# Optimization experiments

Hardware: AMD Instinct MI355X
Metric: run time of the kernel (lower is better)

The kernel has to match this reference:

```python
import jax, jax.numpy as jnp
import numpy as np

B, S, D_IN, D_OUT, H = 4, 2048, 1024, 1024, 16
HD = D_OUT // H  # 64


def setup_inputs() -> dict:
    key = jax.random.key(0)
    ks = jax.random.split(key, 6)
    scale_in = 1.0 / np.sqrt(D_IN)
    scale_out = 1.0 / np.sqrt(D_OUT)
    return {
        "x": jax.random.normal(ks[0], (B, S, D_IN), dtype=jnp.float32),
        "Wq": jax.random.normal(ks[1], (D_IN, D_OUT), dtype=jnp.float32) * scale_in,
        "Wk": jax.random.normal(ks[2], (D_IN, D_OUT), dtype=jnp.float32) * scale_in,
        "Wv": jax.random.normal(ks[3], (D_IN, D_OUT), dtype=jnp.float32) * scale_in,
        "Wo": jax.random.normal(ks[4], (D_OUT, D_OUT), dtype=jnp.float32) * scale_out,
        "bo": jax.random.normal(ks[5], (D_OUT,), dtype=jnp.float32) * 0.01,
    }


def reference(x, Wq, Wk, Wv, Wo, bo):
    b, s, _ = x.shape
    # project and split heads: (b, s, d_out) -> (b, h, s, hd)
    def split(t):
        return t.reshape(b, s, H, HD).transpose(0, 2, 1, 3)
    q = split(x @ Wq)
    k = split(x @ Wk)
    v = split(x @ Wv)
    # scaled causal attention scores (b, h, s, s)
    scores = jnp.einsum('bhqd,bhkd->bhqk', q, k) / jnp.sqrt(jnp.float32(HD))
    causal = jnp.tril(jnp.ones((s, s), dtype=bool))
    scores = jnp.where(causal, scores, -jnp.inf)
    weights = jax.nn.softmax(scores, axis=-1)
    # dropout p=0.0 -> identity (eval mode)
    ctx = jnp.einsum('bhqk,bhkd->bhqd', weights, v)
    ctx = ctx.transpose(0, 2, 1, 3).reshape(b, s, D_OUT)
    return ctx @ Wo + bo
```

## Files before the change

### kernel.cpp

```cpp
#include <hip/hip_runtime.h>
#include <stdint.h>

#define DEVINL __device__ __forceinline__

typedef __attribute__((ext_vector_type(8))) __bf16 bf16x8;
typedef __attribute__((ext_vector_type(4))) float f32x4;
typedef __attribute__((ext_vector_type(8))) unsigned short u16x8;
typedef __attribute__((ext_vector_type(2))) unsigned int u32x2;

constexpr int Bc = 4, Sc = 2048, DINc = 1024, Hc = 16;
constexpr float QSCALE = 0.18033688011112042f;

DEVINL unsigned short f2bf(float x) {
  unsigned u = __builtin_bit_cast(unsigned, x);
  u += 0x7fffu + ((u >> 16) & 1u);
  return (unsigned short)(u >> 16);
}

DEVINL unsigned pack_bf16_trunc(float p0, float p1) {
  return __builtin_amdgcn_perm(__builtin_bit_cast(unsigned, p1),
                               __builtin_bit_cast(unsigned, p0), 0x07060302u);
}

DEVINL void gload_lds16(const void* g, void* l) {
  __builtin_amdgcn_global_load_lds(
      (const __attribute__((address_space(1))) void*)g,
      (__attribute__((address_space(3))) void*)l, 16, 0, 0);
}

template <int ROWS>
DEVINL void stage_tile(const unsigned short* g, int ld, void* lds, int tid) {
#pragma unroll
  for (int p = 0; p < ROWS / 32; ++p) {
    int L = (p * 256 + tid) * 16;
    int row = L >> 7;
    int cb = L & 127;
    int scb = cb ^ ((row & 7) << 4);
    gload_lds16((const char*)(g + (size_t)row * ld) + scb, (char*)lds + L);
  }
}

DEVINL bf16x8 read_frag(const void* lds, int row, int kelem) {
  int addr = row * 128 + (((kelem * 2) ^ ((row & 7) << 4)));
  return *(const bf16x8*)((const char*)lds + addr);
}

__global__ __launch_bounds__(256) void cvt_bf16(const float* __restrict__ in,
                                                unsigned short* __restrict__ out,
                                                int n) {
  int i = (blockIdx.x * 256 + threadIdx.x) * 8;
  if (i + 8 > n) return;
  f32x4 a = *(const f32x4*)(in + i);
  f32x4 b = *(const f32x4*)(in + i + 4);
  u16x8 r;
  r[0] = f2bf(a[0]); r[1] = f2bf(a[1]); r[2] = f2bf(a[2]); r[3] = f2bf(a[3]);
  r[4] = f2bf(b[0]); r[5] = f2bf(b[1]); r[6] = f2bf(b[2]); r[7] = f2bf(b[3]);
  *(u16x8*)(out + i) = r;
}

__global__ __launch_bounds__(256) void transpose_convert4(
    const float* __restrict__ Wq, const float* __restrict__ Wk,
    const float* __restrict__ Wv, const float* __restrict__ Wo,
    unsigned short* __restrict__ wqkvt, unsigned short* __restrict__ wot) {
  __shared__ float t[64][65];
  const float* src;
  unsigned short* dst;
  int z = blockIdx.z;
  if (z == 0)      { src = Wq; dst = wqkvt; }
  else if (z == 1) { src = Wk; dst = wqkvt + (size_t)1024 * 1024; }
  else if (z == 2) { src = Wv; dst = wqkvt + (size_t)2048 * 1024; }
  else             { src = Wo; dst = wot; }
  int n0 = blockIdx.x * 64, k0 = blockIdx.y * 64;
  int tx = threadIdx.x & 63, ty = threadIdx.x >> 6;
#pragma unroll
  for (int r = 0; r < 64; r += 4)
    t[r + ty][tx] = src[(size_t)(k0 + r + ty) * 1024 + n0 + tx];
  __syncthreads();
#pragma unroll
  for (int r = 0; r < 64; r += 4)
    dst[(size_t)(n0 + r + ty) * 1024 + k0 + tx] = f2bf(t[tx][r + ty]);
}

__global__ __launch_bounds__(256, 2) void gemm_qkv(
    const unsigned short* __restrict__ A, const unsigned short* __restrict__ Bt,
    unsigned short* __restrict__ qws, unsigned short* __restrict__ kws,
    unsigned short* __restrict__ vtws) {
  __shared__ __align__(16) unsigned short lA[2][128 * 64];
  __shared__ __align__(16) unsigned short lB[2][128 * 64];
  int tid = threadIdx.x, lane = tid & 63, wave = tid >> 6;
  int wr = wave >> 1, wc = wave & 1;
  int bm = blockIdx.x, bn = blockIdx.y;
  const unsigned short* Ab = A + (size_t)bm * 128 * 1024;
  const unsigned short* Bb = Bt + (size_t)bn * 128 * 1024;
  int r15 = lane & 15, khi = (lane >> 4) * 8;

  f32x4 acc[4][4];
#pragma unroll
  for (int i = 0; i < 4; ++i)
#pragma unroll
    for (int j = 0; j < 4; ++j) acc[i][j] = (f32x4){0.f, 0.f, 0.f, 0.f};

  int cur = 0;
  stage_tile<128>(Ab, 1024, lA[0], tid);
  stage_tile<128>(Bb, 1024, lB[0], tid);
#pragma unroll 1
  for (int t = 0; t < 16; ++t) {
    __syncthreads();
    if (t + 1 < 16) {
      stage_tile<128>(Ab + (t + 1) * 64, 1024, lA[cur ^ 1], tid);
      stage_tile<128>(Bb + (t + 1) * 64, 1024, lB[cur ^ 1], tid);
    }
#pragma unroll
    for (int ks = 0; ks < 2; ++ks) {
      bf16x8 af[4], bfr[4];
#pragma unroll
      for (int i = 0; i < 4; ++i)
        af[i] = read_frag(lA[cur], wr * 64 + i * 16 + r15, ks * 32 + khi);
#pragma unroll
      for (int j = 0; j < 4; ++j)
        bfr[j] = read_frag(lB[cur], wc * 64 + j * 16 + r15, ks * 32 + khi);
      __builtin_amdgcn_s_setprio(1);
#pragma unroll
      for (int i = 0; i < 4; ++i)
#pragma unroll
        for (int j = 0; j < 4; ++j)
          acc[i][j] = __builtin_amdgcn_mfma_f32_16x16x32_bf16(af[i], bfr[j], acc[i][j], 0, 0, 0);
      __builtin_amdgcn_s_setprio(0);
    }
    cur ^= 1;
  }

  int sel = bn >> 3;
  int colbase = (bn & 7) * 128 + wc * 64;
  int mbase = bm * 128 + wr * 64;
#pragma unroll
  for (int i = 0; i < 4; ++i) {
#pragma unroll
    for (int r = 0; r < 4; ++r) {
      int m = mbase + i * 16 + (lane >> 4) * 4 + r;
      int b = m >> 11, s = m & 2047;
#pragma unroll
      for (int j = 0; j < 4; ++j) {
        int col = colbase + j * 16 + r15;
        int h = col >> 6, d = col & 63;
        int bh = b * 16 + h;
        if (sel == 0)
          qws[((size_t)bh * 2048 + s) * 64 + d] = f2bf(acc[i][j][r] * QSCALE);
        else if (sel == 1)
          kws[((size_t)bh * 2048 + s) * 64 + d] = f2bf(acc[i][j][r]);
        else
          vtws[((size_t)bh * 64 + d) * 2048 + s] = f2bf(acc[i][j][r]);
      }
    }
  }
}

__global__ __launch_bounds__(256, 3) void attn(
    const unsigned short* __restrict__ qws, const unsigned short* __restrict__ kws,
    const unsigned short* __restrict__ vtws, unsigned short* __restrict__ ctx) {
  __shared__ __align__(16) unsigned short lK[2][64 * 64];
  __shared__ __align__(16) unsigned short lV[2][64 * 64];
  __shared__ __align__(16) unsigned short lP[4][32 * 64];
  int tid = threadIdx.x, lane = tid & 63, wave = tid >> 6;
  int lid = blockIdx.x + 8 * blockIdx.y;
  int bh = (lid & 7) * 8 + ((lid >> 3) & 7);
  int pairid = lid >> 6;
  int r15 = lane & 15, g4 = lane >> 4;
  const unsigned short* Kb = kws + (size_t)bh * 2048 * 64;
  const unsigned short* Vb = vtws + (size_t)bh * 64 * 2048;
  int b = bh >> 4, h = bh & 15;
  char* Pw = (char*)&lP[wave][0];

#pragma unroll 1
  for (int seg = 0; seg < 2; ++seg) {
    int t = seg == 0 ? (15 - pairid) : pairid;
    int q0 = t * 128;
    int myrow0 = q0 + wave * 32;
    const unsigned short* Qb = qws + ((size_t)bh * 2048 + myrow0) * 64;

    bf16x8 qf[2][2];
#pragma unroll
    for (int mf = 0; mf < 2; ++mf)
#pragma unroll
      for (int ks = 0; ks < 2; ++ks)
        qf[mf][ks] = *(const bf16x8*)(Qb + (size_t)(mf * 16 + r15) * 64 + ks * 32 + g4 * 8);

    float m_run[2] = {-1e30f, -1e30f}, l_run[2] = {0.f, 0.f};
    f32x4 o_acc[2][4];
#pragma unroll
    for (int mf = 0; mf < 2; ++mf)
#pragma unroll
      for (int df = 0; df < 4; ++df) o_acc[mf][df] = (f32x4){0.f, 0.f, 0.f, 0.f};

    int nkt = 2 * t + 2;
    __syncthreads();
    int cur = 0;
    stage_tile<64>(Kb, 64, lK[0], tid);
    stage_tile<64>(Vb, 2048, lV[0], tid);

#pragma unroll 1
    for (int kt = 0; kt < nkt; ++kt) {
      __syncthreads();
      if (kt + 1 < nkt) {
        stage_tile<64>(Kb + (size_t)(kt + 1) * 64 * 64, 64, lK[cur ^ 1], tid);
        stage_tile<64>(Vb + (size_t)(kt + 1) * 64, 2048, lV[cur ^ 1], tid);
      }

      f32x4 sacc[2][4];
#pragma unroll
      for (int mf = 0; mf < 2; ++mf)
#pragma unroll
        for (int nf = 0; nf < 4; ++nf) sacc[mf][nf] = (f32x4){0.f, 0.f, 0.f, 0.f};
#pragma unroll
      for (int ks = 0; ks < 2; ++ks) {
        bf16x8 kf[4];
#pragma unroll
        for (int nf = 0; nf < 4; ++nf)
          kf[nf] = read_frag(lK[cur], nf * 16 + r15, ks * 32 + g4 * 8);
        __builtin_amdgcn_s_setprio(1);
#pragma unroll
        for (int mf = 0; mf < 2; ++mf)
#pragma unroll
          for (int nf = 0; nf < 4; ++nf)
            sacc[mf][nf] = __builtin_amdgcn_mfma_f32_16x16x32_bf16(kf[nf], qf[mf][ks], sacc[mf][nf], 0, 0, 0);
        __builtin_amdgcn_s_setprio(0);
      }

      if (kt * 64 + 63 > myrow0) {
#pragma unroll
        for (int mf = 0; mf < 2; ++mf) {
          int q = myrow0 + mf * 16 + r15;
#pragma unroll
          for (int nf = 0; nf < 4; ++nf) {
            int kbase = kt * 64 + nf * 16 + g4 * 4;
#pragma unroll
            for (int r = 0; r < 4; ++r)
              if (kbase + r > q) sacc[mf][nf][r] = -3e38f;
          }
        }
      }

      float tm[2];
#pragma unroll
      for (int mf = 0; mf < 2; ++mf) {
        float a0 = fmaxf(fmaxf(sacc[mf][0][0], sacc[mf][0][1]), fmaxf(sacc[mf][0][2], sacc[mf][0][3]));
        float a1 = fmaxf(fmaxf(sacc[mf][1][0], sacc[mf][1][1]), fmaxf(sacc[mf][1][2], sacc[mf][1][3]));
        float a2 = fmaxf(fmaxf(sacc[mf][2][0], sacc[mf][2][1]), fmaxf(sacc[mf][2][2], sacc[mf][2][3]));
        float a3 = fmaxf(fmaxf(sacc[mf][3][0], sacc[mf][3][1]), fmaxf(sacc[mf][3][2], sacc[mf][3][3]));
        float m = fmaxf(fmaxf(a0, a1), fmaxf(a2, a3));
        m = fmaxf(m, __shfl_xor(m, 16));
        m = fmaxf(m, __shfl_xor(m, 32));
        tm[mf] = m;
      }

      bool ok = (tm[0] <= m_run[0] + 11.5f) & (tm[1] <= m_run[1] + 11.5f);
      if (!__all(ok)) {
#pragma unroll
        for (int mf = 0; mf < 2; ++mf) {
          float mn = fmaxf(m_run[mf], tm[mf]);
          float a = __builtin_amdgcn_exp2f(m_run[mf] - mn);
          m_run[mf] = mn;
          l_run[mf] *= a;
          float av[4];
#pragma unroll
          for (int r = 0; r < 4; ++r)
            av[r] = __shfl(a, (g4 * 4 + r) | (lane & 48));
#pragma unroll
          for (int df = 0; df < 4; ++df)
#pragma unroll
            for (int r = 0; r < 4; ++r) o_acc[mf][df][r] *= av[r];
        }
      }

      float rs[2] = {0.f, 0.f};
#pragma unroll
      for (int mf = 0; mf < 2; ++mf) {
        int prow = mf * 16 + r15;
        char* Prow = Pw + prow * 128;
        int sw = (prow & 7) << 4;
#pragma unroll
        for (int nf = 0; nf < 4; ++nf) {
          float p0 = __builtin_amdgcn_exp2f(sacc[mf][nf][0] - m_run[mf]);
          float p1 = __builtin_amdgcn_exp2f(sacc[mf][nf][1] - m_run[mf]);
          float p2 = __builtin_amdgcn_exp2f(sacc[mf][nf][2] - m_run[mf]);
          float p3 = __builtin_amdgcn_exp2f(sacc[mf][nf][3] - m_run[mf]);
          rs[mf] += (p0 + p1) + (p2 + p3);
          *(u32x2*)(Prow + (((nf * 16 + g4 * 4) * 2) ^ sw)) =
              (u32x2){pack_bf16_trunc(p0, p1), pack_bf16_trunc(p2, p3)};
        }
        float s = rs[mf];
        s += __shfl_xor(s, 16);
        s += __shfl_xor(s, 32);
        l_run[mf] += s;
      }

#pragma unroll
      for (int ks = 0; ks < 2; ++ks) {
        bf16x8 vf[4];
#pragma unroll
        for (int df = 0; df < 4; ++df)
          vf[df] = read_frag(lV[cur], df * 16 + r15, ks * 32 + g4 * 8);
        bf16x8 pf[2];
#pragma unroll
        for (int mf = 0; mf < 2; ++mf)
          pf[mf] = read_frag(Pw, mf * 16 + r15, ks * 32 + g4 * 8);
        __builtin_amdgcn_s_setprio(1);
#pragma unroll
        for (int mf = 0; mf < 2; ++mf)
#pragma unroll
          for (int df = 0; df < 4; ++df)
            o_acc[mf][df] = __builtin_amdgcn_mfma_f32_16x16x32_bf16(pf[mf], vf[df], o_acc[mf][df], 0, 0, 0);
        __builtin_amdgcn_s_setprio(0);
      }
      cur ^= 1;
    }

#pragma unroll
    for (int mf = 0; mf < 2; ++mf) {
      float rl = 1.f / l_run[mf];
      float rv[4];
#pragma unroll
      for (int r = 0; r < 4; ++r)
        rv[r] = __shfl(rl, (g4 * 4 + r) | (lane & 48));
#pragma unroll
      for (int r = 0; r < 4; ++r) {
        int row = myrow0 + mf * 16 + g4 * 4 + r;
#pragma unroll
        for (int df = 0; df < 4; ++df)
          ctx[((size_t)(b * 2048 + row)) * 1024 + h * 64 + df * 16 + r15] =
              f2bf(o_acc[mf][df][r] * rv[r]);
      }
    }
  }
}

__global__ __launch_bounds__(256, 2) void gemm_out(
    const unsigned short* __restrict__ A, const unsigned short* __restrict__ Bt,
    const float* __restrict__ bo, float* __restrict__ out) {
  __shared__ __align__(16) unsigned short lA[2][128 * 64];
  __shared__ __align__(16) unsigned short lB[2][128 * 64];
  int tid = threadIdx.x, lane = tid & 63, wave = tid >> 6;
  int wr = wave >> 1, wc = wave & 1;
  int bm = blockIdx.x, bn = blockIdx.y;
  const unsigned short* Ab = A + (size_t)bm * 128 * 1024;
  const unsigned short* Bb = Bt + (size_t)bn * 128 * 1024;
  int r15 = lane & 15, khi = (lane >> 4) * 8;

  f32x4 acc[4][4];
#pragma unroll
  for (int i = 0; i < 4; ++i)
#pragma unroll
    for (int j = 0; j < 4; ++j) acc[i][j] = (f32x4){0.f, 0.f, 0.f, 0.f};

  int cur = 0;
  stage_tile<128>(Ab, 1024, lA[0], tid);
  stage_tile<128>(Bb, 1024, lB[0], tid);
#pragma unroll 1
  for (int t = 0; t < 16; ++t) {
    __syncthreads();
    if (t + 1 < 16) {
      stage_tile<128>(Ab + (t + 1) * 64, 1024, lA[cur ^ 1], tid);
      stage_tile<128>(Bb + (t + 1) * 64, 1024, lB[cur ^ 1], tid);
    }
#pragma unroll
    for (int ks = 0; ks < 2; ++ks) {
      bf16x8 af[4], bfr[4];
#pragma unroll
      for (int i = 0; i < 4; ++i)
        af[i] = read_frag(lA[cur], wr * 64 + i * 16 + r15, ks * 32 + khi);
#pragma unroll
      for (int j = 0; j < 4; ++j)
        bfr[j] = read_frag(lB[cur], wc * 64 + j * 16 + r15, ks * 32 + khi);
      __builtin_amdgcn_s_setprio(1);
#pragma unroll
      for (int i = 0; i < 4; ++i)
#pragma unroll
        for (int j = 0; j < 4; ++j)
          acc[i][j] = __builtin_amdgcn_mfma_f32_16x16x32_bf16(af[i], bfr[j], acc[i][j], 0, 0, 0);
      __builtin_amdgcn_s_setprio(0);
    }
    cur ^= 1;
  }

  int nbase = bn * 128 + wc * 64;
  int mbase = bm * 128 + wr * 64;
#pragma unroll
  for (int j = 0; j < 4; ++j) {
    int n = nbase + j * 16 + r15;
    float bias = bo[n];
#pragma unroll
    for (int i = 0; i < 4; ++i)
#pragma unroll
      for (int r = 0; r < 4; ++r) {
        int m = mbase + i * 16 + (lane >> 4) * 4 + r;
        out[(size_t)m * 1024 + n] = acc[i][j][r] + bias;
      }
  }
}

extern "C" void kernel_launch(void* const* d_in, const int* in_sizes, int n_in,
                              void* d_out, int out_size, void* d_ws, size_t ws_size,
                              hipStream_t stream) {
  const float* x = (const float*)d_in[0];
  const float* Wq = (const float*)d_in[1];
  const float* Wk = (const float*)d_in[2];
  const float* Wv = (const float*)d_in[3];
  const float* Wo = (const float*)d_in[4];
  const float* bo = (const float*)d_in[5];
  float* out = (float*)d_out;

  char* ws = (char*)d_ws;
  unsigned short* xb    = (unsigned short*)(ws);
  unsigned short* wqkvt = (unsigned short*)(ws + (16u << 20));
  unsigned short* wot   = (unsigned short*)(ws + (22u << 20));
  unsigned short* qws   = (unsigned short*)(ws + (24u << 20));
  unsigned short* kws   = (unsigned short*)(ws + (40u << 20));
  unsigned short* vtws  = (unsigned short*)(ws + (56u << 20));
  unsigned short* ctxws = (unsigned short*)(ws + (72u << 20));

  cvt_bf16<<<dim3(4096), dim3(256), 0, stream>>>(x, xb, Bc * Sc * DINc);
  transpose_convert4<<<dim3(16, 16, 4), dim3(256), 0, stream>>>(Wq, Wk, Wv, Wo, wqkvt, wot);

  gemm_qkv<<<dim3(64, 24), dim3(256), 0, stream>>>(xb, wqkvt, qws, kws, vtws);
  attn<<<dim3(8, 64), dim3(256), 0, stream>>>(qws, kws, vtws, ctxws);
  gemm_out<<<dim3(64, 8), dim3(256), 0, stream>>>(ctxws, wot, bo, out);
}
```

Measured before the change: 177.0 us.

## Enlarge QKV and output GEMM tiles to 256-row blocks with 512 threads

Both projection GEMMs now use 512-thread blocks with larger block tiles: 256x256 for the QKV projection and 256x128 for the output projection. The staging helper is generalised to take the thread count. The larger tiles raise data reuse per LDS load and cut global traffic. In exchange, LDS use per block grows (128 KB for QKV), which may limit occupancy, and there are fewer blocks to spread across the CUs.

```diff
diff --git a/kernel.cpp b/kernel.cpp
--- a/kernel.cpp
+++ b/kernel.cpp
@@ -28,11 +28,11 @@
       (__attribute__((address_space(3))) void*)l, 16, 0, 0);
 }
 
-template <int ROWS>
+template <int ROWS, int THREADS>
 DEVINL void stage_tile(const unsigned short* g, int ld, void* lds, int tid) {
 #pragma unroll
-  for (int p = 0; p < ROWS / 32; ++p) {
-    int L = (p * 256 + tid) * 16;
+  for (int p = 0; p < (ROWS * 128) / (THREADS * 16); ++p) {
+    int L = (p * THREADS + tid) * 16;
     int row = L >> 7;
     int cb = L & 127;
     int scb = cb ^ ((row & 7) << 4);
@@ -81,63 +81,62 @@
     dst[(size_t)(n0 + r + ty) * 1024 + k0 + tx] = f2bf(t[tx][r + ty]);
 }
 
-__global__ __launch_bounds__(256, 2) void gemm_qkv(
+__global__ __launch_bounds__(512, 2) void gemm_qkv(
     const unsigned short* __restrict__ A, const unsigned short* __restrict__ Bt,
     unsigned short* __restrict__ qws, unsigned short* __restrict__ kws,
     unsigned short* __restrict__ vtws) {
-  __shared__ __align__(16) unsigned short lA[2][128 * 64];
-  __shared__ __align__(16) unsigned short lB[2][128 * 64];
+  __shared__ __align__(16) unsigned short lA[2][256 * 64];
+  __shared__ __align__(16) unsigned short lB[2][256 * 64];
   int tid = threadIdx.x, lane = tid & 63, wave = tid >> 6;
-  int wr = wave >> 1, wc = wave & 1;
+  int wr = wave >> 2, wc = wave & 3;
   int bm = blockIdx.x, bn = blockIdx.y;
-  const unsigned short* Ab = A + (size_t)bm * 128 * 1024;
-  const unsigned short* Bb = Bt + (size_t)bn * 128 * 1024;
-  int r15 = lane & 15, khi = (lane >> 4) * 8;
-
-  f32x4 acc[4][4];
-#pragma unroll
-  for (int i = 0; i < 4; ++i)
+  const unsigned short* Ab = A + (size_t)bm * 256 * 1024;
+  const unsigned short* Bb = Bt + (size_t)bn * 256 * 1024;
+  int r15 = lane & 15, g4 = lane >> 4, khi = g4 * 8;
+
+  f32x4 acc[8][4];
+#pragma unroll
+  for (int i = 0; i < 8; ++i)
 #pragma unroll
     for (int j = 0; j < 4; ++j) acc[i][j] = (f32x4){0.f, 0.f, 0.f, 0.f};
 
   int cur = 0;
-  stage_tile<128>(Ab, 1024, lA[0], tid);
-  stage_tile<128>(Bb, 1024, lB[0], tid);
+  stage_tile<256, 512>(Ab, 1024, lA[0], tid);
+  stage_tile<256, 512>(Bb, 1024, lB[0], tid);
 #pragma unroll 1
   for (int t = 0; t < 16; ++t) {
     __syncthreads();
     if (t + 1 < 16) {
-      stage_tile<128>(Ab + (t + 1) * 64, 1024, lA[cur ^ 1], tid);
-      stage_tile<128>(Bb + (t + 1) * 64, 1024, lB[cur ^ 1], tid);
+      stage_tile<256, 512>(Ab + (t + 1) * 64, 1024, lA[cur ^ 1], tid);
+      stage_tile<256, 512>(Bb + (t + 1) * 64, 1024, lB[cur ^ 1], tid);
     }
 #pragma unroll
     for (int ks = 0; ks < 2; ++ks) {
-      bf16x8 af[4], bfr[4];
-#pragma unroll
-      for (int i = 0; i < 4; ++i)
-        af[i] = read_frag(lA[cur], wr * 64 + i * 16 + r15, ks * 32 + khi);
+      bf16x8 bfr[4];
 #pragma unroll
       for (int j = 0; j < 4; ++j)
         bfr[j] = read_frag(lB[cur], wc * 64 + j * 16 + r15, ks * 32 + khi);
-      __builtin_amdgcn_s_setprio(1);
-#pragma unroll
-      for (int i = 0; i < 4; ++i)
+#pragma unroll
+      for (int i = 0; i < 8; ++i) {
+        bf16x8 af = read_frag(lA[cur], wr * 128 + i * 16 + r15, ks * 32 + khi);
+        __builtin_amdgcn_s_setprio(1);
 #pragma unroll
         for (int j = 0; j < 4; ++j)
-          acc[i][j] = __builtin_amdgcn_mfma_f32_16x16x32_bf16(af[i], bfr[j], acc[i][j], 0, 0, 0);
-      __builtin_amdgcn_s_setprio(0);
+          acc[i][j] = __builtin_amdgcn_mfma_f32_16x16x32_bf16(af, bfr[j], acc[i][j], 0, 0, 0);
+        __builtin_amdgcn_s_setprio(0);
+      }
     }
     cur ^= 1;
   }
 
-  int sel = bn >> 3;
-  int colbase = (bn & 7) * 128 + wc * 64;
-  int mbase = bm * 128 + wr * 64;
-#pragma unroll
-  for (int i = 0; i < 4; ++i) {
+  int sel = bn >> 2;
+  int colbase = (bn & 3) * 256 + wc * 64;
+  int mbase = bm * 256 + wr * 128;
+#pragma unroll
+  for (int i = 0; i < 8; ++i) {
 #pragma unroll
     for (int r = 0; r < 4; ++r) {
-      int m = mbase + i * 16 + (lane >> 4) * 4 + r;
+      int m = mbase + i * 16 + g4 * 4 + r;
       int b = m >> 11, s = m & 2047;
 #pragma unroll
       for (int j = 0; j < 4; ++j) {
@@ -195,15 +194,15 @@
     int nkt = 2 * t + 2;
     __syncthreads();
     int cur = 0;
-    stage_tile<64>(Kb, 64, lK[0], tid);
-    stage_tile<64>(Vb, 2048, lV[0], tid);
+    stage_tile<64, 256>(Kb, 64, lK[0], tid);
+    stage_tile<64, 256>(Vb, 2048, lV[0], tid);
 
 #pragma unroll 1
     for (int kt = 0; kt < nkt; ++kt) {
       __syncthreads();
       if (kt + 1 < nkt) {
-        stage_tile<64>(Kb + (size_t)(kt + 1) * 64 * 64, 64, lK[cur ^ 1], tid);
-        stage_tile<64>(Vb + (size_t)(kt + 1) * 64, 2048, lV[cur ^ 1], tid);
+        stage_tile<64, 256>(Kb + (size_t)(kt + 1) * 64 * 64, 64, lK[cur ^ 1], tid);
+        stage_tile<64, 256>(Vb + (size_t)(kt + 1) * 64, 2048, lV[cur ^ 1], tid);
       }
 
       f32x4 sacc[2][4];
@@ -334,17 +333,17 @@
   }
 }
 
-__global__ __launch_bounds__(256, 2) void gemm_out(
+__global__ __launch_bounds__(512, 2) void gemm_out(
     const unsigned short* __restrict__ A, const unsigned short* __restrict__ Bt,
     const float* __restrict__ bo, float* __restrict__ out) {
-  __shared__ __align__(16) unsigned short lA[2][128 * 64];
+  __shared__ __align__(16) unsigned short lA[2][256 * 64];
   __shared__ __align__(16) unsigned short lB[2][128 * 64];
   int tid = threadIdx.x, lane = tid & 63, wave = tid >> 6;
   int wr = wave >> 1, wc = wave & 1;
   int bm = blockIdx.x, bn = blockIdx.y;
-  const unsigned short* Ab = A + (size_t)bm * 128 * 1024;
+  const unsigned short* Ab = A + (size_t)bm * 256 * 1024;
   const unsigned short* Bb = Bt + (size_t)bn * 128 * 1024;
-  int r15 = lane & 15, khi = (lane >> 4) * 8;
+  int r15 = lane & 15, g4 = lane >> 4, khi = g4 * 8;
 
   f32x4 acc[4][4];
 #pragma unroll
@@ -353,14 +352,14 @@
     for (int j = 0; j < 4; ++j) acc[i][j] = (f32x4){0.f, 0.f, 0.f, 0.f};
 
   int cur = 0;
-  stage_tile<128>(Ab, 1024, lA[0], tid);
-  stage_tile<128>(Bb, 1024, lB[0], tid);
+  stage_tile<256, 512>(Ab, 1024, lA[0], tid);
+  stage_tile<128, 512>(Bb, 1024, lB[0], tid);
 #pragma unroll 1
   for (int t = 0; t < 16; ++t) {
     __syncthreads();
     if (t + 1 < 16) {
-      stage_tile<128>(Ab + (t + 1) * 64, 1024, lA[cur ^ 1], tid);
-      stage_tile<128>(Bb + (t + 1) * 64, 1024, lB[cur ^ 1], tid);
+      stage_tile<256, 512>(Ab + (t + 1) * 64, 1024, lA[cur ^ 1], tid);
+      stage_tile<128, 512>(Bb + (t + 1) * 64, 1024, lB[cur ^ 1], tid);
     }
 #pragma unroll
     for (int ks = 0; ks < 2; ++ks) {
@@ -383,7 +382,7 @@
   }
 
   int nbase = bn * 128 + wc * 64;
-  int mbase = bm * 128 + wr * 64;
+  int mbase = bm * 256 + wr * 64;
 #pragma unroll
   for (int j = 0; j < 4; ++j) {
     int n = nbase + j * 16 + r15;
@@ -392,7 +391,7 @@
     for (int i = 0; i < 4; ++i)
 #pragma unroll
       for (int r = 0; r < 4; ++r) {
-        int m = mbase + i * 16 + (lane >> 4) * 4 + r;
+        int m = mbase + i * 16 + g4 * 4 + r;
         out[(size_t)m * 1024 + n] = acc[i][j][r] + bias;
       }
   }
@@ -421,7 +420,7 @@
   cvt_bf16<<<dim3(4096), dim3(256), 0, stream>>>(x, xb, Bc * Sc * DINc);
   transpose_convert4<<<dim3(16, 16, 4), dim3(256), 0, stream>>>(Wq, Wk, Wv, Wo, wqkvt, wot);
 
-  gemm_qkv<<<dim3(64, 24), dim3(256), 0, stream>>>(xb, wqkvt, qws, kws, vtws);
+  gemm_qkv<<<dim3(32, 12), dim3(512), 0, stream>>>(xb, wqkvt, qws, kws, vtws);
   attn<<<dim3(8, 64), dim3(256), 0, stream>>>(qws, kws, vtws, ctxws);
-  gemm_out<<<dim3(64, 8), dim3(256), 0, stream>>>(ctxws, wot, bo, out);
-}
+  gemm_out<<<dim3(32, 8), dim3(512), 0, stream>>>(ctxws, wot, bo, out);
+}
```

After: 207.6 us. 1.17x slower.
